# Kernel optimization log

Hardware: AMD Instinct MI355X
Metric: run time of the kernel (lower is better)

## Reference

```python
import jax, jax.numpy as jnp
import numpy as np

B, T, H = 4096, 512, 256


def setup_inputs() -> dict:
    key = jax.random.key(0)
    ks = jax.random.split(key, 10)
    s = 0.05
    return {
        "x": jax.random.normal(ks[0], (B, T, 1), dtype=jnp.float32),
        "eps": jax.random.normal(ks[1], (B, T, 1), dtype=jnp.float32),  # randn_like noise, pregenerated
        "w_ih": jax.random.normal(ks[2], (4 * H, 1), dtype=jnp.float32) * s,
        "w_hh": jax.random.normal(ks[3], (4 * H, H), dtype=jnp.float32) * s,
        "b_ih": jax.random.normal(ks[4], (4 * H,), dtype=jnp.float32) * s,
        "b_hh": jax.random.normal(ks[5], (4 * H,), dtype=jnp.float32) * s,
        "w_mean": jax.random.normal(ks[6], (1, H), dtype=jnp.float32) * s,
        "b_mean": jax.random.normal(ks[7], (1,), dtype=jnp.float32) * s,
        "w_logvar": jax.random.normal(ks[8], (1, H), dtype=jnp.float32) * s,
        "b_logvar": jax.random.normal(ks[9], (1,), dtype=jnp.float32) * s,
    }


def reference(x, eps, w_ih, w_hh, b_ih, b_hh, w_mean, b_mean, w_logvar, b_logvar):
    """Teacher-forcing forward: per-step LSTMCell + mean/logvar heads + reparam sample.
    Returns (outputs, means, logvars), each [B, T, 1]."""
    b = x.shape[0]
    h0 = jnp.zeros((b, H), dtype=x.dtype)
    c0 = jnp.zeros((b, H), dtype=x.dtype)

    def step(carry, inp):
        h, c = carry
        xt, et = inp  # [B,1] each
        # PyTorch LSTMCell: gates ordered (i, f, g, o)
        gates = xt @ w_ih.T + b_ih + h @ w_hh.T + b_hh  # [B, 4H]
        i, f, g, o = jnp.split(gates, 4, axis=-1)
        i = jax.nn.sigmoid(i)
        f = jax.nn.sigmoid(f)
        g = jnp.tanh(g)
        o = jax.nn.sigmoid(o)
        c = f * c + i * g
        h = o * jnp.tanh(c)
        mean = h @ w_mean.T + b_mean            # [B, 1]
        logvar = jnp.clip(h @ w_logvar.T + b_logvar, -10.0, 2.0)
        sample = mean + jnp.exp(0.5 * logvar) * et
        return (h, c), (sample, mean, logvar)

    xs = (jnp.swapaxes(x, 0, 1), jnp.swapaxes(eps, 0, 1))  # time-major [T,B,1]
    _, (s, m, lv) = jax.lax.scan(step, (h0, c0), xs)
    to_bt = lambda a: jnp.swapaxes(a, 0, 1)  # back to [B,T,1]
    return to_bt(s), to_bt(m), to_bt(lv)
```

## Files before the change

kernel.cpp:

```cpp
#include <hip/hip_runtime.h>
#include <hip/hip_bf16.h>

#define BB 4096
#define TT 512
#define HH 256

typedef __bf16 bf16x8 __attribute__((ext_vector_type(8)));
typedef __bf16 bf16x4 __attribute__((ext_vector_type(4)));
typedef float f32x4 __attribute__((ext_vector_type(4)));
typedef int i32x8 __attribute__((ext_vector_type(8)));
typedef long fp8frag;

#define MFMA_BF16 __builtin_amdgcn_mfma_f32_16x16x32_bf16
#define MFMA_FP8  __builtin_amdgcn_mfma_f32_16x16x32_fp8_fp8
#define MFMA_SC(A, B, C) \
    __builtin_amdgcn_mfma_scale_f32_16x16x128_f8f6f4( \
        A, B, C, 0, 0, 0, 0x7F7F7F7F, 0, 0x7F7F7F7F)

#if defined(__has_builtin)
#if __has_builtin(__builtin_amdgcn_exp2f)
#define EXP2F(x) __builtin_amdgcn_exp2f(x)
#endif
#endif
#ifndef EXP2F
#define EXP2F(x) __expf((x) * 0.6931471805599453f)
#endif
#define RCPF(x) __builtin_amdgcn_rcpf(x)

#define L2E  1.4426950408889634f
#define TL2E 2.8853900817779268f
#define HL2E 0.7213475204444817f

__global__ void prep_weights8(const float* __restrict__ w_hh, const float* __restrict__ w_ih,
                              const float* __restrict__ b_ih, const float* __restrict__ b_hh,
                              char* __restrict__ wB8) {
    int idx = blockIdx.x * blockDim.x + threadIdx.x;
    if (idx < 64 * 2 * 64) {
        int l = idx & 63;
        int kb = (idx >> 6) & 1;
        int ctg = idx >> 7;
        int n = ctg * 16 + (l & 15);
        int k0 = kb * 128 + (l >> 4) * 32;
        const float* src = w_hh + n * HH + k0;
        i32x8 v;
#pragma unroll
        for (int d = 0; d < 8; ++d) {
            int pk = __builtin_amdgcn_cvt_pk_fp8_f32(src[4 * d] * 64.f,
                                                     src[4 * d + 1] * 64.f, 0, false);
            pk = __builtin_amdgcn_cvt_pk_fp8_f32(src[4 * d + 2] * 64.f,
                                                 src[4 * d + 3] * 64.f, pk, true);
            v[d] = pk;
        }
        *(i32x8*)(wB8 + (size_t)idx * 32) = v;
    } else if (idx < 64 * 2 * 64 + 64 * 64) {
        int j = idx - 64 * 2 * 64;
        int l = j & 63;
        int ctg = j >> 6;
        int n = ctg * 16 + (l & 15);
        int k0 = 256 + 8 * (l >> 4);
        float f[8];
#pragma unroll
        for (int e = 0; e < 8; ++e) {
            int k = k0 + e;
            float v = 0.f;
            if (k == 256) v = w_ih[n];
            else if (k == 257) v = b_ih[n] + b_hh[n];
            f[e] = v * 64.f;
        }
        int lo = __builtin_amdgcn_cvt_pk_fp8_f32(f[0], f[1], 0, false);
        lo = __builtin_amdgcn_cvt_pk_fp8_f32(f[2], f[3], lo, true);
        int hi = __builtin_amdgcn_cvt_pk_fp8_f32(f[4], f[5], 0, false);
        hi = __builtin_amdgcn_cvt_pk_fp8_f32(f[6], f[7], hi, true);
        int2 v2; v2.x = lo; v2.y = hi;
        *(int2*)(wB8 + 262144 + (size_t)j * 8) = v2;
    }
}

__global__ __launch_bounds__(512, 1) void lstm_fused(
    const float* __restrict__ x, const float* __restrict__ eps,
    const float* __restrict__ w_mean, const float* __restrict__ b_mean,
    const float* __restrict__ w_logvar, const float* __restrict__ b_logvar,
    const char* __restrict__ wB8, float* __restrict__ out)
{
    __shared__ __align__(16) __bf16 hbuf[2][16][296];
    __shared__ __align__(16) char hbuf8[2][16][304];
    __shared__ __align__(16) __bf16 headw[9][512];
    __shared__ float obuf[2][16][16];

    const int tid = threadIdx.x;
    const int w = tid >> 6;
    const int l = tid & 63;
    const int m0 = blockIdx.x * 16;

    for (int i = tid; i < 2 * 16 * 296; i += 512) (&hbuf[0][0][0])[i] = (__bf16)0.f;
    for (int i = tid; i < 2 * 16 * 304; i += 512) (&hbuf8[0][0][0])[i] = 0;
    for (int i = tid; i < 9 * 64; i += 512) {
        int kt = i >> 6, hl = i & 63;
        int col = hl & 15;
        int k0 = kt * 32 + 8 * (hl >> 4);
        bf16x8 hw;
#pragma unroll
        for (int e = 0; e < 8; ++e) {
            int k = k0 + e;
            float v = 0.f;
            if (k < 256) {
                if (col == 0) v = w_mean[k];
                else if (col == 1) v = w_logvar[k];
            } else if (k == 257) {
                if (col == 0) v = b_mean[0];
                else if (col == 1) v = b_logvar[0];
            }
            hw[e] = (__bf16)v;
        }
        *(bf16x8*)&headw[kt][hl * 8] = hw;
    }

    i32x8 wbig[16];
    fp8frag wsm[8];
#pragma unroll
    for (int cc = 0; cc < 8; ++cc) {
        const int ctg = w + 8 * (cc >> 2) + 16 * (cc & 3);
        wbig[2 * cc]     = *(const i32x8*)(wB8 + ((size_t)(ctg * 2 + 0) * 64 + l) * 32);
        wbig[2 * cc + 1] = *(const i32x8*)(wB8 + ((size_t)(ctg * 2 + 1) * 64 + l) * 32);
        wsm[cc] = *(const fp8frag*)(wB8 + 262144 + ((size_t)ctg * 64 + l) * 8);
    }

    const int arow = l & 15;
    const int a32 = 32 * (l >> 4);
    const int ak8 = 8 * (l >> 4);
    const int ako = 16 * (l >> 4);
    const int u0 = 16 * w + ((l >> 4) << 2);
    const int u1 = u0 + 128;

    const float DS1c = L2E / 1024.f;
    const float DS2c = TL2E / 1024.f;

    float c[8];
#pragma unroll
    for (int i = 0; i < 8; ++i) c[i] = 0.f;
    const f32x4 Z = {0.f, 0.f, 0.f, 0.f};

    __syncthreads();
    if (tid < 16) {
        hbuf[0][tid][257] = (__bf16)1.0f;
        hbuf[1][tid][257] = (__bf16)1.0f;
        hbuf8[0][tid][257] = (char)__builtin_amdgcn_cvt_pk_fp8_f32(16.f, 0.f, 0, false);
        hbuf8[1][tid][257] = (char)__builtin_amdgcn_cvt_pk_fp8_f32(16.f, 0.f, 0, false);
        float x0 = x[(size_t)(m0 + tid) * TT];
        hbuf[1][tid][256] = (__bf16)x0;
        hbuf8[1][tid][256] = (char)__builtin_amdgcn_cvt_pk_fp8_f32(x0 * 16.f, 0.f, 0, false);
    }
    __syncthreads();

#define PAIR(SA, SB, DST)                                                       \
    do {                                                                        \
        float sb_ = fminf((SB), 80.f);                                          \
        float e1_ = EXP2F(-(SA)), e2_ = EXP2F(sb_);                             \
        DST = (e2_ - 1.f) * RCPF((1.f + e1_) * (1.f + e2_));                    \
    } while (0)

#define EWAC(J)                                                                 \
    do {                                                                        \
        float ig_, h_;                                                          \
        PAIR(a0[J] * DS1c, a2[J] * DS2c, ig_);                                  \
        float fg_ = RCPF(1.f + EXP2F(-(a1[J] * DS1c)));                         \
        float cn_ = fmaf(fg_, c[J], ig_);                                       \
        c[J] = cn_;                                                             \
        PAIR(a3[J] * DS1c, cn_ * TL2E, h_);                                     \
        hA[J] = h_;                                                             \
    } while (0)

#define EWBC(J)                                                                 \
    do {                                                                        \
        float ig_, h_;                                                          \
        PAIR(a4[J] * DS1c, a6[J] * DS2c, ig_);                                  \
        float fg_ = RCPF(1.f + EXP2F(-(a5[J] * DS1c)));                         \
        float cn_ = fmaf(fg_, c[4 + (J)], ig_);                                 \
        c[4 + (J)] = cn_;                                                       \
        PAIR(a7[J] * DS1c, cn_ * TL2E, h_);                                     \
        hB[J] = h_;                                                             \
    } while (0)

#define WRH(PB, HV, U)                                                          \
    do {                                                                        \
        bf16x4 hb_ = {(__bf16)HV[0], (__bf16)HV[1], (__bf16)HV[2], (__bf16)HV[3]};\
        *(bf16x4*)&hbuf[PB][arow][U] = hb_;                                     \
        int pk_ = __builtin_amdgcn_cvt_pk_fp8_f32(HV[0] * 16.f, HV[1] * 16.f, 0, false);\
        pk_ = __builtin_amdgcn_cvt_pk_fp8_f32(HV[2] * 16.f, HV[3] * 16.f, pk_, true);  \
        *(int*)&hbuf8[PB][arow][U] = pk_;                                       \
    } while (0)

#define HEADS(RB, SLOT)                                                         \
    do {                                                                        \
        f32x4 ah_;                                                              \
        {                                                                       \
            bf16x8 hb_ = *(const bf16x8*)&hbuf[RB][arow][0 * 32 + ako / 2];     \
            ah_ = MFMA_BF16(*(const bf16x8*)&headw[0][l * 8], hb_, Z, 0, 0, 0); \
        }                                                                       \
        _Pragma("unroll")                                                       \
        for (int kt_ = 1; kt_ < 9; ++kt_) {                                     \
            bf16x8 hb_ = *(const bf16x8*)&hbuf[RB][arow][kt_ * 32 + ako / 2];   \
            ah_ = MFMA_BF16(*(const bf16x8*)&headw[kt_][l * 8], hb_, ah_, 0, 0, 0);\
        }                                                                       \
        if (l < 16) {                                                           \
            obuf[0][l][SLOT] = ah_[0];                                          \
            obuf[1][l][SLOT] = fminf(fmaxf(ah_[1], -10.f), 2.f);                \
        }                                                                       \
    } while (0)

#define FLUSH(T0)                                                               \
    do {                                                                        \
        if (tid < 192) {                                                        \
            const int o_ = tid >> 6, rr_ = (tid >> 2) & 15, q_ = tid & 3;       \
            f32x4 mv_ = *(const f32x4*)&obuf[0][rr_][q_ * 4];                   \
            f32x4 lv_ = *(const f32x4*)&obuf[1][rr_][q_ * 4];                   \
            const size_t base_ = (size_t)(m0 + rr_) * TT + (T0) + q_ * 4;       \
            if (o_ == 0) {                                                      \
                f32x4 e_ = *(const f32x4*)&eps[base_];                          \
                f32x4 s_;                                                       \
                _Pragma("unroll")                                               \
                for (int k_ = 0; k_ < 4; ++k_)                                  \
                    s_[k_] = fmaf(EXP2F(lv_[k_] * HL2E), e_[k_], mv_[k_]);      \
                *(f32x4*)&out[base_] = s_;                                      \
            } else if (o_ == 1) {                                               \
                *(f32x4*)&out[(size_t)BB * TT + base_] = mv_;                   \
            } else {                                                            \
                *(f32x4*)&out[2 * (size_t)BB * TT + base_] = lv_;               \
            }                                                                   \
        }                                                                       \
    } while (0)

#define STEP(PB, RB)                                                            \
    do {                                                                        \
        const int tt = t0 + (PB);                                               \
        float xn = 0.f;                                                         \
        if (tid < 16 && tt + 1 < TT) xn = x[(size_t)(m0 + tid) * TT + (tt + 1)];\
        i32x8 hf0 = *(const i32x8*)&hbuf8[RB][arow][a32];                       \
        i32x8 hf1 = *(const i32x8*)&hbuf8[RB][arow][128 + a32];                 \
        fp8frag hf8 = *(const fp8frag*)&hbuf8[RB][arow][256 + ak8];             \
        f32x4 a0, a1, a2, a3, a4, a5, a6, a7;                                   \
        float hA[4], hB[4];                                                     \
                                           \
        a0 = MFMA_SC(wbig[0], hf0, Z);  a1 = MFMA_SC(wbig[2], hf0, Z);          \
        a2 = MFMA_SC(wbig[4], hf0, Z);  a3 = MFMA_SC(wbig[6], hf0, Z);          \
        a0 = MFMA_SC(wbig[1], hf1, a0); a1 = MFMA_SC(wbig[3], hf1, a1);         \
        a2 = MFMA_SC(wbig[5], hf1, a2); a3 = MFMA_SC(wbig[7], hf1, a3);         \
        a0 = MFMA_FP8(wsm[0], hf8, a0, 0, 0, 0);                                \
        a1 = MFMA_FP8(wsm[1], hf8, a1, 0, 0, 0);                                \
        a2 = MFMA_FP8(wsm[2], hf8, a2, 0, 0, 0);                                \
        a3 = MFMA_FP8(wsm[3], hf8, a3, 0, 0, 0);                                \
                         \
        a4 = MFMA_SC(wbig[8], hf0, Z);  a5 = MFMA_SC(wbig[10], hf0, Z);         \
        a6 = MFMA_SC(wbig[12], hf0, Z); a7 = MFMA_SC(wbig[14], hf0, Z);         \
        EWAC(0);                                                                \
        a4 = MFMA_SC(wbig[9], hf1, a4); a5 = MFMA_SC(wbig[11], hf1, a5);        \
        EWAC(1);                                                                \
        a6 = MFMA_SC(wbig[13], hf1, a6); a7 = MFMA_SC(wbig[15], hf1, a7);       \
        EWAC(2);                                                                \
        a4 = MFMA_FP8(wsm[4], hf8, a4, 0, 0, 0);                                \
        a5 = MFMA_FP8(wsm[5], hf8, a5, 0, 0, 0);                                \
        a6 = MFMA_FP8(wsm[6], hf8, a6, 0, 0, 0);                                \
        a7 = MFMA_FP8(wsm[7], hf8, a7, 0, 0, 0);                                \
        EWAC(3);                                                                \
        WRH(PB, hA, u0);                                                        \
        if (w == 7 && tt >= 1) { HEADS(RB, (tt - 1) & 15); }                    \
        EWBC(0); EWBC(1); EWBC(2); EWBC(3);                                     \
        WRH(PB, hB, u1);                                                        \
        if (tid < 16 && tt + 1 < TT) {                                          \
            hbuf[PB][tid][256] = (__bf16)xn;                                    \
            hbuf8[PB][tid][256] =                                               \
                (char)__builtin_amdgcn_cvt_pk_fp8_f32(xn * 16.f, 0.f, 0, false);\
        }                                                                       \
        if ((PB) == 0 && tt > 0 && (tt & 15) == 0) {                            \
            __syncthreads();                                                    \
            FLUSH(tt - 16);                                                     \
        }                                                                       \
        __syncthreads();                                                        \
    } while (0)

    for (int t0 = 0; t0 < TT; t0 += 2) {
        STEP(0, 1);
        STEP(1, 0);
    }

    if (w == 7) { HEADS(1, 15); }
    __syncthreads();
    FLUSH(TT - 16);

#undef PAIR
#undef EWAC
#undef EWBC
#undef WRH
#undef HEADS
#undef FLUSH
#undef STEP
}

extern "C" void kernel_launch(void* const* d_in, const int* in_sizes, int n_in,
                              void* d_out, int out_size, void* d_ws, size_t ws_size,
                              hipStream_t stream) {
    const float* x = (const float*)d_in[0];
    const float* eps = (const float*)d_in[1];
    const float* w_ih = (const float*)d_in[2];
    const float* w_hh = (const float*)d_in[3];
    const float* b_ih = (const float*)d_in[4];
    const float* b_hh = (const float*)d_in[5];
    const float* w_mean = (const float*)d_in[6];
    const float* b_mean = (const float*)d_in[7];
    const float* w_logvar = (const float*)d_in[8];
    const float* b_logvar = (const float*)d_in[9];

    char* wB8 = (char*)d_ws;

    prep_weights8<<<48, 256, 0, stream>>>(w_hh, w_ih, b_ih, b_hh, wB8);
    lstm_fused<<<256, 512, 0, stream>>>(x, eps, w_mean, b_mean, w_logvar, b_logvar,
                                        wB8, (float*)d_out);
}
```

Measured before the change: 885.2 us.

## Software-pipeline first-half recurrent MFMAs of next step under current gate math

Splits each step's recurrent matmul by K half. The first-half MFMAs for the next timestep run on the freshly written h (u0 part), right after a new mid-step barrier, and are interleaved with the second-half gate elementwise work of the current step. Accumulators ping-pong between two register arrays across steps. The goal is to hide MFMA latency on the serial recurrence critical path, at the cost of an extra __syncthreads per step and more live accumulator registers.

```diff
diff --git a/kernel.cpp b/kernel.cpp
--- a/kernel.cpp
+++ b/kernel.cpp
@@ -159,25 +159,25 @@
         DST = (e2_ - 1.f) * RCPF((1.f + e1_) * (1.f + e2_));                    \
     } while (0)
 
-#define EWAC(J)                                                                 \
+#define EWAC(CU, J)                                                             \
     do {                                                                        \
         float ig_, h_;                                                          \
-        PAIR(a0[J] * DS1c, a2[J] * DS2c, ig_);                                  \
-        float fg_ = RCPF(1.f + EXP2F(-(a1[J] * DS1c)));                         \
+        PAIR(CU[0][J] * DS1c, CU[2][J] * DS2c, ig_);                            \
+        float fg_ = RCPF(1.f + EXP2F(-(CU[1][J] * DS1c)));                      \
         float cn_ = fmaf(fg_, c[J], ig_);                                       \
         c[J] = cn_;                                                             \
-        PAIR(a3[J] * DS1c, cn_ * TL2E, h_);                                     \
+        PAIR(CU[3][J] * DS1c, cn_ * TL2E, h_);                                  \
         hA[J] = h_;                                                             \
     } while (0)
 
-#define EWBC(J)                                                                 \
+#define EWBC(CU, J)                                                             \
     do {                                                                        \
         float ig_, h_;                                                          \
-        PAIR(a4[J] * DS1c, a6[J] * DS2c, ig_);                                  \
-        float fg_ = RCPF(1.f + EXP2F(-(a5[J] * DS1c)));                         \
+        PAIR(CU[4][J] * DS1c, CU[6][J] * DS2c, ig_);                            \
+        float fg_ = RCPF(1.f + EXP2F(-(CU[5][J] * DS1c)));                      \
         float cn_ = fmaf(fg_, c[4 + (J)], ig_);                                 \
         c[4 + (J)] = cn_;                                                       \
-        PAIR(a7[J] * DS1c, cn_ * TL2E, h_);                                     \
+        PAIR(CU[7][J] * DS1c, cn_ * TL2E, h_);                                  \
         hB[J] = h_;                                                             \
     } while (0)
 
@@ -230,41 +230,42 @@
         }                                                                       \
     } while (0)
 
-#define STEP(PB, RB)                                                            \
+#define STEP(PB, RB, CU, NX)                                                    \
     do {                                                                        \
         const int tt = t0 + (PB);                                               \
         float xn = 0.f;                                                         \
         if (tid < 16 && tt + 1 < TT) xn = x[(size_t)(m0 + tid) * TT + (tt + 1)];\
-        i32x8 hf0 = *(const i32x8*)&hbuf8[RB][arow][a32];                       \
         i32x8 hf1 = *(const i32x8*)&hbuf8[RB][arow][128 + a32];                 \
         fp8frag hf8 = *(const fp8frag*)&hbuf8[RB][arow][256 + ak8];             \
-        f32x4 a0, a1, a2, a3, a4, a5, a6, a7;                                   \
         float hA[4], hB[4];                                                     \
-                                           \
-        a0 = MFMA_SC(wbig[0], hf0, Z);  a1 = MFMA_SC(wbig[2], hf0, Z);          \
-        a2 = MFMA_SC(wbig[4], hf0, Z);  a3 = MFMA_SC(wbig[6], hf0, Z);          \
-        a0 = MFMA_SC(wbig[1], hf1, a0); a1 = MFMA_SC(wbig[3], hf1, a1);         \
-        a2 = MFMA_SC(wbig[5], hf1, a2); a3 = MFMA_SC(wbig[7], hf1, a3);         \
-        a0 = MFMA_FP8(wsm[0], hf8, a0, 0, 0, 0);                                \
-        a1 = MFMA_FP8(wsm[1], hf8, a1, 0, 0, 0);                                \
-        a2 = MFMA_FP8(wsm[2], hf8, a2, 0, 0, 0);                                \
-        a3 = MFMA_FP8(wsm[3], hf8, a3, 0, 0, 0);                                \
-                         \
-        a4 = MFMA_SC(wbig[8], hf0, Z);  a5 = MFMA_SC(wbig[10], hf0, Z);         \
-        a6 = MFMA_SC(wbig[12], hf0, Z); a7 = MFMA_SC(wbig[14], hf0, Z);         \
-        EWAC(0);                                                                \
-        a4 = MFMA_SC(wbig[9], hf1, a4); a5 = MFMA_SC(wbig[11], hf1, a5);        \
-        EWAC(1);                                                                \
-        a6 = MFMA_SC(wbig[13], hf1, a6); a7 = MFMA_SC(wbig[15], hf1, a7);       \
-        EWAC(2);                                                                \
-        a4 = MFMA_FP8(wsm[4], hf8, a4, 0, 0, 0);                                \
-        a5 = MFMA_FP8(wsm[5], hf8, a5, 0, 0, 0);                                \
-        a6 = MFMA_FP8(wsm[6], hf8, a6, 0, 0, 0);                                \
-        a7 = MFMA_FP8(wsm[7], hf8, a7, 0, 0, 0);                                \
-        EWAC(3);                                                                \
+                  \
+        CU[0] = MFMA_SC(wbig[1],  hf1, CU[0]);  CU[1] = MFMA_SC(wbig[3],  hf1, CU[1]); \
+        CU[2] = MFMA_SC(wbig[5],  hf1, CU[2]);  CU[3] = MFMA_SC(wbig[7],  hf1, CU[3]); \
+        CU[4] = MFMA_SC(wbig[9],  hf1, CU[4]);  CU[5] = MFMA_SC(wbig[11], hf1, CU[5]); \
+        CU[6] = MFMA_SC(wbig[13], hf1, CU[6]);  CU[7] = MFMA_SC(wbig[15], hf1, CU[7]); \
+        CU[0] = MFMA_FP8(wsm[0], hf8, CU[0], 0, 0, 0);                          \
+        CU[1] = MFMA_FP8(wsm[1], hf8, CU[1], 0, 0, 0);                          \
+        CU[2] = MFMA_FP8(wsm[2], hf8, CU[2], 0, 0, 0);                          \
+        CU[3] = MFMA_FP8(wsm[3], hf8, CU[3], 0, 0, 0);                          \
+        CU[4] = MFMA_FP8(wsm[4], hf8, CU[4], 0, 0, 0);                          \
+        CU[5] = MFMA_FP8(wsm[5], hf8, CU[5], 0, 0, 0);                          \
+        CU[6] = MFMA_FP8(wsm[6], hf8, CU[6], 0, 0, 0);                          \
+        CU[7] = MFMA_FP8(wsm[7], hf8, CU[7], 0, 0, 0);                          \
+                                       \
+        EWAC(CU, 0); EWAC(CU, 1); EWAC(CU, 2); EWAC(CU, 3);                     \
         WRH(PB, hA, u0);                                                        \
         if (w == 7 && tt >= 1) { HEADS(RB, (tt - 1) & 15); }                    \
-        EWBC(0); EWBC(1); EWBC(2); EWBC(3);                                     \
+        __syncthreads();                    \
+                         \
+        i32x8 hf0n = *(const i32x8*)&hbuf8[PB][arow][a32];                      \
+        NX[0] = MFMA_SC(wbig[0],  hf0n, Z);  NX[1] = MFMA_SC(wbig[2],  hf0n, Z);\
+        EWBC(CU, 0);                                                            \
+        NX[2] = MFMA_SC(wbig[4],  hf0n, Z);  NX[3] = MFMA_SC(wbig[6],  hf0n, Z);\
+        EWBC(CU, 1);                                                            \
+        NX[4] = MFMA_SC(wbig[8],  hf0n, Z);  NX[5] = MFMA_SC(wbig[10], hf0n, Z);\
+        EWBC(CU, 2);                                                            \
+        NX[6] = MFMA_SC(wbig[12], hf0n, Z);  NX[7] = MFMA_SC(wbig[14], hf0n, Z);\
+        EWBC(CU, 3);                                                            \
         WRH(PB, hB, u1);                                                        \
         if (tid < 16 && tt + 1 < TT) {                                          \
             hbuf[PB][tid][256] = (__bf16)xn;                                    \
@@ -275,12 +276,16 @@
             __syncthreads();                                                    \
             FLUSH(tt - 16);                                                     \
         }                                                                       \
-        __syncthreads();                                                        \
-    } while (0)
+        __syncthreads();                \
+    } while (0)
+
+    f32x4 accA[8], accB[8];
+#pragma unroll
+    for (int i = 0; i < 8; ++i) accA[i] = Z;
 
     for (int t0 = 0; t0 < TT; t0 += 2) {
-        STEP(0, 1);
-        STEP(1, 0);
+        STEP(0, 1, accA, accB);
+        STEP(1, 0, accB, accA);
     }
 
     if (w == 7) { HEADS(1, 15); }
```

New measurement: 896.8 us. About the same (+1.3%).
